# Performance work log

Hardware: AMD Instinct MI355X
Metric: run time of the kernel (lower is better)

The kernel has to match this reference:

```python
import jax, jax.numpy as jnp
import numpy as np

D_MODEL = 512
D_STATE = 16
EPS = 1e-8
LN_EPS = 1e-5


def setup_inputs() -> dict:
    key = jax.random.key(0)
    ks = jax.random.split(key, 9)
    B, N = 4, 2048
    x = jax.random.normal(ks[0], (B, N, D_MODEL), dtype=jnp.float32)
    A_log = jax.random.normal(ks[1], (D_STATE,), dtype=jnp.float32) * 0.1 - 1.0
    # xavier_uniform with gain=0.5 for B and C linear weights
    lim_B = 0.5 * np.sqrt(6.0 / (D_MODEL + D_STATE))
    W_B = jax.random.uniform(ks[2], (D_STATE, D_MODEL), jnp.float32, -lim_B, lim_B)
    W_C = jax.random.uniform(ks[3], (D_MODEL, D_STATE), jnp.float32, -lim_B, lim_B)
    D = jax.random.normal(ks[4], (D_MODEL,), dtype=jnp.float32) * 0.01
    lim_g = np.sqrt(1.0 / D_MODEL)  # torch Linear default init
    W_gate = jax.random.uniform(ks[5], (D_MODEL, D_MODEL), jnp.float32, -lim_g, lim_g)
    b_gate = jax.random.uniform(ks[6], (D_MODEL,), jnp.float32, -lim_g, lim_g)
    ln_gamma = jnp.ones((D_MODEL,), jnp.float32)
    ln_beta = jnp.zeros((D_MODEL,), jnp.float32)
    return {"x": x, "A_log": A_log, "W_B": W_B, "W_C": W_C, "D": D,
            "W_gate": W_gate, "b_gate": b_gate, "ln_gamma": ln_gamma, "ln_beta": ln_beta}


def reference(x, A_log, W_B, W_C, D, W_gate, b_gate, ln_gamma, ln_beta):
    Bb, N, Dm = x.shape
    A = -jnp.clip(jnp.exp(A_log), EPS, 10.0)                      # (d_state,)
    dt = 1.0 / N
    A_bar = jnp.exp(dt * A)                                       # (d_state,)
    B_bar = jnp.where(jnp.abs(A) > EPS, (A_bar - 1.0) / (A + EPS),
                      jnp.full_like(A, dt))
    Bu = jnp.einsum('bnm,sm->bns', x, W_B) * B_bar                # (B,N,d_state)
    idx = jnp.arange(N)
    diff = jnp.clip(idx[None, :] - idx[:, None], 0, None)[..., None]  # (N,N,1)
    decay = A_bar[None, None, :] ** diff                          # (N,N,d_state)
    mask = (idx[None, :] >= idx[:, None])[..., None]
    decay = decay * mask.astype(decay.dtype)
    h = jnp.einsum('nms,bns->bms', decay, Bu)                     # (B,N,d_state)
    h = jnp.clip(h, -10.0, 10.0)
    y = jnp.einsum('bns,ms->bnm', h, W_C) + D * x                 # (B,N,d_model)
    gate = jax.nn.sigmoid(jnp.einsum('bnm,km->bnk', x, W_gate) + b_gate)
    y = gate * y + (1.0 - gate) * x
    # LayerNorm (dropout is identity in eval mode)
    mu = jnp.mean(y, axis=-1, keepdims=True)
    var = jnp.var(y, axis=-1, keepdims=True)
    return (y - mu) / jnp.sqrt(var + LN_EPS) * ln_gamma + ln_beta
```

## Files before the change

kernel.cpp:

```cpp
#include <hip/hip_runtime.h>
#include <math.h>
#include <stdint.h>

#define D_MODEL 512
#define D_STATE 16
#define NSEQ    2048
#define NBATCH  4
#define EPSF    1e-8f
#define LN_EPSF 1e-5f
#define DT      (1.0f / 2048.0f)

typedef __attribute__((ext_vector_type(8))) short short8;
typedef __attribute__((ext_vector_type(4))) float floatx4;

__device__ __forceinline__ ushort f2bf(float f) {
    uint32_t u = __float_as_uint(f);
    return (ushort)((u + 0x7fffu + ((u >> 16) & 1u)) >> 16);
}

__global__ __launch_bounds__(256) void kP(const float* __restrict__ x,
                                          const float* __restrict__ A_log,
                                          const float* __restrict__ W_B,
                                          const float* __restrict__ Wg,
                                          ushort* __restrict__ wgb,
                                          float* __restrict__ hL,
                                          float* __restrict__ states) {
    __shared__ float wb[D_STATE][D_MODEL + 4];
    __shared__ float bbars[16], abars[16];
    __shared__ float w4[4][16];
    const int tid = threadIdx.x, lane = tid & 63, wave = tid >> 6;

    if (tid < 64) {
        int i = blockIdx.x * 64 + tid;
        const float4* sp = (const float4*)Wg + (size_t)i * 2;
        float4 a = sp[0], b = sp[1];
        float v[8] = {a.x, a.y, a.z, a.w, b.x, b.y, b.z, b.w};
        short8 o;
        #pragma unroll
        for (int j = 0; j < 8; ++j) o[j] = (short)f2bf(v[j]);
        *(short8*)(wgb + (size_t)i * 8) = o;
    }
    if (tid < 16) {
        float A    = -fminf(fmaxf(expf(A_log[tid]), EPSF), 10.0f);
        float Abar = expf(A * DT);
        abars[tid] = Abar;
        bbars[tid] = (fabsf(A) > EPSF) ? (Abar - 1.0f) / (A + EPSF) : DT;
    }
    __syncthreads();
    for (int i = tid; i < D_STATE * D_MODEL; i += 256) {
        int s = i >> 9, m = i & 511;
        wb[s][m] = W_B[i] * bbars[s];
    }
    __syncthreads();

    const int s    = lane & 15;
    const int q    = lane >> 4;
    const int rloc = q + (wave << 2);
    const int row  = blockIdx.x * 16 + rloc;
    const float* xr = x + (size_t)row * D_MODEL;

    float acc = 0.f;
    #pragma unroll 4
    for (int m = 0; m < D_MODEL; m += 4) {
        float4 xv = *(const float4*)(xr + m);
        float4 wv = *(const float4*)(&wb[s][m]);
        acc += xv.x * wv.x + xv.y * wv.y + xv.z * wv.z + xv.w * wv.w;
    }

    float abar = abars[s];
    float a = abar, b = acc;
    {
        float ap = __shfl_up(a, 16), bp = __shfl_up(b, 16);
        if (lane >= 16) { b = a * bp + b; a = a * ap; }
    }
    {
        float ap = __shfl_up(a, 32), bp = __shfl_up(b, 32);
        if (lane >= 32) { b = a * bp + b; a = a * ap; }
    }
    if (q == 3) w4[wave][s] = b;
    __syncthreads();
    float a4 = abar * abar; a4 = a4 * a4;
    float pb = 0.f;
    for (int w = 0; w < wave; ++w) pb = a4 * pb + w4[w][s];
    float hloc = a * pb + b;

    hL[(size_t)row * D_STATE + s] = hloc;
    if (rloc == 15) states[(size_t)blockIdx.x * D_STATE + s] = hloc;
}

#define CBM 16
#define BKC 64
__global__ __launch_bounds__(256) void kc_fused(
    const float*  __restrict__ x,
    const ushort* __restrict__ Wg,
    const float*  __restrict__ hL,
    const float*  __restrict__ states,
    const float*  __restrict__ A_log,
    const float*  __restrict__ W_C,
    const float*  __restrict__ Dvec,
    const float*  __restrict__ bg,
    const float*  __restrict__ gamma,
    const float*  __restrict__ beta,
    float* __restrict__ out) {
    __shared__ ushort Bsub[512 * BKC];
    __shared__ float  hsf[CBM][D_STATE];
    __shared__ float  red[4][CBM][2];

    const int tid  = threadIdx.x;
    const int lane = tid & 63, wave = tid >> 6;
    const int r0   = blockIdx.x * CBM;
    const int fr   = lane & 15, kg = lane >> 4;
    const int colw = wave * 128;

    short8 afp[8][2];
    #pragma unroll
    for (int t = 0; t < 8; ++t) {
        const float* ap = x + (size_t)(r0 + fr) * D_MODEL + t * 64 + kg * 8;
        float4 u0 = *(const float4*)ap;
        float4 u1 = *(const float4*)(ap + 4);
        float4 v0 = *(const float4*)(ap + 32);
        float4 v1 = *(const float4*)(ap + 36);
        float uu[8] = {u0.x,u0.y,u0.z,u0.w,u1.x,u1.y,u1.z,u1.w};
        float vv[8] = {v0.x,v0.y,v0.z,v0.w,v1.x,v1.y,v1.z,v1.w};
        #pragma unroll
        for (int e = 0; e < 8; ++e) {
            afp[t][0][e] = (short)f2bf(uu[e]);
            afp[t][1][e] = (short)f2bf(vv[e]);
        }
    }

    float* stg = (float*)Bsub;
    const int c0 = blockIdx.x & 127;
    for (int i = tid; i < c0 * 16; i += 256)
        stg[i] = states[(size_t)(blockIdx.x - c0) * 16 + i];
    __syncthreads();
    {
        int s = tid & 15, nloc = tid >> 4;
        float A   = -fminf(fmaxf(expf(A_log[s]), EPSF), 10.0f);
        float a16 = expf(A * DT * 16.0f);
        float p = 0.f;
        for (int cc = 0; cc < c0; ++cc) p = a16 * p + stg[cc * 16 + s];
        float hv = expf(A * DT * (float)(nloc + 1)) * p
                 + hL[(size_t)(r0 + nloc) * D_STATE + s];
        hsf[nloc][s] = fminf(fmaxf(hv, -10.f), 10.f);
    }

    floatx4 acc[8] = {};
    #pragma unroll
    for (int t = 0; t < 8; ++t) {
        __syncthreads();
        #pragma unroll
        for (int is = 0; is < 16; ++is) {
            int row_ = is * 32 + (tid >> 3);
            int g_   = (tid & 7) ^ (row_ & 7);
            const ushort* gsrc_ = Wg + (size_t)row_ * D_MODEL + t * 64 + g_ * 8;
            __builtin_amdgcn_global_load_lds(
                (const __attribute__((address_space(1))) void*)gsrc_,
                (__attribute__((address_space(3))) void*)((char*)Bsub + is * 4096 + tid * 16),
                16, 0, 0);
        }
        __syncthreads();

        #pragma unroll
        for (int j = 0; j < 8; ++j) {
            int rb = colw + j * 16 + fr;
            short8 b0 = *(const short8*)(Bsub + (size_t)rb * BKC + (((kg    ) ^ (rb & 7)) * 8));
            short8 b1 = *(const short8*)(Bsub + (size_t)rb * BKC + (((kg + 4) ^ (rb & 7)) * 8));
            acc[j] = __builtin_amdgcn_mfma_f32_16x16x32_bf16(afp[t][0], b0, acc[j], 0, 0, 0);
            acc[j] = __builtin_amdgcn_mfma_f32_16x16x32_bf16(afp[t][1], b1, acc[j], 0, 0, 0);
        }
    }

    float vsum[4] = {}, vsq[4] = {};
    #pragma unroll
    for (int j = 0; j < 8; ++j) {
        int col = colw + j * 16 + fr;
        float dv = Dvec[col], bgv = bg[col];
        const float4* wcp = (const float4*)(W_C + (size_t)col * D_STATE);
        float4 w0 = wcp[0], w1 = wcp[1], w2 = wcp[2], w3 = wcp[3];
        #pragma unroll
        for (int q = 0; q < 4; ++q) {
            int rl = kg * 4 + q;
            float xv = x[(size_t)(r0 + rl) * D_MODEL + col];
            const float* hp = hsf[rl];
            float yv = dv * xv
                + hp[0]*w0.x + hp[1]*w0.y + hp[2]*w0.z + hp[3]*w0.w
                + hp[4]*w1.x + hp[5]*w1.y + hp[6]*w1.z + hp[7]*w1.w
                + hp[8]*w2.x + hp[9]*w2.y + hp[10]*w2.z + hp[11]*w2.w
                + hp[12]*w3.x + hp[13]*w3.y + hp[14]*w3.z + hp[15]*w3.w;
            float lg = acc[j][q] + bgv;
            float gt = 1.f / (1.f + expf(-lg));
            float v  = gt * yv + (1.f - gt) * xv;
            acc[j][q] = v;
            vsum[q] += v;
            vsq[q]  += v * v;
        }
    }
    #pragma unroll
    for (int off = 1; off < 16; off <<= 1) {
        #pragma unroll
        for (int q = 0; q < 4; ++q) {
            vsum[q] += __shfl_xor(vsum[q], off);
            vsq[q]  += __shfl_xor(vsq[q], off);
        }
    }
    if (fr == 0) {
        #pragma unroll
        for (int q = 0; q < 4; ++q) {
            red[wave][kg * 4 + q][0] = vsum[q];
            red[wave][kg * 4 + q][1] = vsq[q];
        }
    }
    __syncthreads();
    float mu[4], rs[4];
    #pragma unroll
    for (int q = 0; q < 4; ++q) {
        int rl = kg * 4 + q;
        float s = 0.f, ss = 0.f;
        #pragma unroll
        for (int w = 0; w < 4; ++w) { s += red[w][rl][0]; ss += red[w][rl][1]; }
        float m   = s * (1.f / (float)D_MODEL);
        float var = ss * (1.f / (float)D_MODEL) - m * m;
        mu[q] = m;
        rs[q] = rsqrtf(var + LN_EPSF);
    }
    #pragma unroll
    for (int j = 0; j < 8; ++j) {
        int col = colw + j * 16 + fr;
        float ga = gamma[col], be = beta[col];
        #pragma unroll
        for (int q = 0; q < 4; ++q)
            out[(size_t)(r0 + kg * 4 + q) * D_MODEL + col] =
                (acc[j][q] - mu[q]) * rs[q] * ga + be;
    }
}

extern "C" void kernel_launch(void* const* d_in, const int* in_sizes, int n_in,
                              void* d_out, int out_size, void* d_ws, size_t ws_size,
                              hipStream_t stream) {
    const float* x     = (const float*)d_in[0];
    const float* A_log = (const float*)d_in[1];
    const float* W_B   = (const float*)d_in[2];
    const float* W_C   = (const float*)d_in[3];
    const float* Dv    = (const float*)d_in[4];
    const float* Wg    = (const float*)d_in[5];
    const float* bg    = (const float*)d_in[6];
    const float* gamma = (const float*)d_in[7];
    const float* beta  = (const float*)d_in[8];
    float* out = (float*)d_out;

    const int rows = NBATCH * NSEQ;

    ushort* wgb    = (ushort*)d_ws;
    float*  hL     = (float*)(wgb + (size_t)D_MODEL * D_MODEL);
    float*  states = hL + (size_t)rows * D_STATE;

    hipLaunchKernelGGL(kP, dim3(rows / 16), dim3(256), 0, stream,
                       x, A_log, W_B, Wg, wgb, hL, states);
    hipLaunchKernelGGL(kc_fused, dim3(rows / CBM), dim3(256), 0, stream,
                       x, wgb, hL, states, A_log, W_C, Dv, bg, gamma, beta, out);
}
```

Measured before the change: 58.55 us.

## Double row tile per block to share W_gate LDS tiles across 8 waves

The fused gate/LayerNorm kernel now handles 32 rows per block with 512 threads, and two groups of four waves share each W_gate bf16 tile staged in LDS. This halves the total number of W_gate tile loads from global/L2 across the grid and halves the block count. The cross-chunk state prefix and the LayerNorm reduction indexing are reworked to cover two 16-row chunks per block. In exchange there are fewer blocks (256), larger blocks with more synchronisation cost, and possibly lower occupancy.

After: 50.40 us. -13.9%, faster.

```diff
diff --git a/kernel.cpp b/kernel.cpp
--- a/kernel.cpp
+++ b/kernel.cpp
@@ -88,9 +88,9 @@
     if (rloc == 15) states[(size_t)blockIdx.x * D_STATE + s] = hloc;
 }
 
-#define CBM 16
+#define CBM 32
 #define BKC 64
-__global__ __launch_bounds__(256) void kc_fused(
+__global__ __launch_bounds__(512) void kc_fused(
     const float*  __restrict__ x,
     const ushort* __restrict__ Wg,
     const float*  __restrict__ hL,
@@ -104,18 +104,19 @@
     float* __restrict__ out) {
     __shared__ ushort Bsub[512 * BKC];
     __shared__ float  hsf[CBM][D_STATE];
-    __shared__ float  red[4][CBM][2];
+    __shared__ float  red[8][CBM][2];
 
     const int tid  = threadIdx.x;
     const int lane = tid & 63, wave = tid >> 6;
     const int r0   = blockIdx.x * CBM;
     const int fr   = lane & 15, kg = lane >> 4;
-    const int colw = wave * 128;
+    const int rbase = r0 + (wave >> 2) * 16;
+    const int colw  = (wave & 3) * 128;
 
     short8 afp[8][2];
     #pragma unroll
     for (int t = 0; t < 8; ++t) {
-        const float* ap = x + (size_t)(r0 + fr) * D_MODEL + t * 64 + kg * 8;
+        const float* ap = x + (size_t)(rbase + fr) * D_MODEL + t * 64 + kg * 8;
         float4 u0 = *(const float4*)ap;
         float4 u1 = *(const float4*)(ap + 4);
         float4 v0 = *(const float4*)(ap + 32);
@@ -130,17 +131,19 @@
     }
 
     float* stg = (float*)Bsub;
-    const int c0 = blockIdx.x & 127;
-    for (int i = tid; i < c0 * 16; i += 256)
-        stg[i] = states[(size_t)(blockIdx.x - c0) * 16 + i];
+    const int c0    = (blockIdx.x & 63) * 2;
+    const int cbase = (blockIdx.x >> 6) * 128;
+    for (int i = tid; i < (c0 + 1) * 16; i += 512)
+        stg[i] = states[(size_t)cbase * 16 + i];
     __syncthreads();
     {
         int s = tid & 15, nloc = tid >> 4;
         float A   = -fminf(fmaxf(expf(A_log[s]), EPSF), 10.0f);
         float a16 = expf(A * DT * 16.0f);
+        int nch = c0 + (nloc >> 4);
         float p = 0.f;
-        for (int cc = 0; cc < c0; ++cc) p = a16 * p + stg[cc * 16 + s];
-        float hv = expf(A * DT * (float)(nloc + 1)) * p
+        for (int cc = 0; cc < nch; ++cc) p = a16 * p + stg[cc * 16 + s];
+        float hv = expf(A * DT * (float)((nloc & 15) + 1)) * p
                  + hL[(size_t)(r0 + nloc) * D_STATE + s];
         hsf[nloc][s] = fminf(fmaxf(hv, -10.f), 10.f);
     }
@@ -150,13 +153,13 @@
     for (int t = 0; t < 8; ++t) {
         __syncthreads();
         #pragma unroll
-        for (int is = 0; is < 16; ++is) {
-            int row_ = is * 32 + (tid >> 3);
+        for (int is = 0; is < 8; ++is) {
+            int row_ = is * 64 + (tid >> 3);
             int g_   = (tid & 7) ^ (row_ & 7);
             const ushort* gsrc_ = Wg + (size_t)row_ * D_MODEL + t * 64 + g_ * 8;
             __builtin_amdgcn_global_load_lds(
                 (const __attribute__((address_space(1))) void*)gsrc_,
-                (__attribute__((address_space(3))) void*)((char*)Bsub + is * 4096 + tid * 16),
+                (__attribute__((address_space(3))) void*)((char*)Bsub + is * 8192 + tid * 16),
                 16, 0, 0);
         }
         __syncthreads();
@@ -180,9 +183,9 @@
         float4 w0 = wcp[0], w1 = wcp[1], w2 = wcp[2], w3 = wcp[3];
         #pragma unroll
         for (int q = 0; q < 4; ++q) {
-            int rl = kg * 4 + q;
-            float xv = x[(size_t)(r0 + rl) * D_MODEL + col];
-            const float* hp = hsf[rl];
+            int rloc = (wave >> 2) * 16 + kg * 4 + q;
+            float xv = x[(size_t)(r0 + rloc) * D_MODEL + col];
+            const float* hp = hsf[rloc];
             float yv = dv * xv
                 + hp[0]*w0.x + hp[1]*w0.y + hp[2]*w0.z + hp[3]*w0.w
                 + hp[4]*w1.x + hp[5]*w1.y + hp[6]*w1.z + hp[7]*w1.w
@@ -207,18 +210,23 @@
     if (fr == 0) {
         #pragma unroll
         for (int q = 0; q < 4; ++q) {
-            red[wave][kg * 4 + q][0] = vsum[q];
-            red[wave][kg * 4 + q][1] = vsq[q];
+            int rloc = (wave >> 2) * 16 + kg * 4 + q;
+            red[wave][rloc][0] = vsum[q];
+            red[wave][rloc][1] = vsq[q];
         }
     }
     __syncthreads();
     float mu[4], rs[4];
     #pragma unroll
     for (int q = 0; q < 4; ++q) {
-        int rl = kg * 4 + q;
+        int rloc = (wave >> 2) * 16 + kg * 4 + q;
+        int wg0  = (wave >> 2) * 4;
         float s = 0.f, ss = 0.f;
         #pragma unroll
-        for (int w = 0; w < 4; ++w) { s += red[w][rl][0]; ss += red[w][rl][1]; }
+        for (int w = 0; w < 4; ++w) {
+            s  += red[wg0 + w][rloc][0];
+            ss += red[wg0 + w][rloc][1];
+        }
         float m   = s * (1.f / (float)D_MODEL);
         float var = ss * (1.f / (float)D_MODEL) - m * m;
         mu[q] = m;
@@ -229,9 +237,11 @@
         int col = colw + j * 16 + fr;
         float ga = gamma[col], be = beta[col];
         #pragma unroll
-        for (int q = 0; q < 4; ++q)
-            out[(size_t)(r0 + kg * 4 + q) * D_MODEL + col] =
+        for (int q = 0; q < 4; ++q) {
+            int rloc = (wave >> 2) * 16 + kg * 4 + q;
+            out[(size_t)(r0 + rloc) * D_MODEL + col] =
                 (acc[j][q] - mu[q]) * rs[q] * ga + be;
+        }
     }
 }
 
@@ -257,6 +267,6 @@
 
     hipLaunchKernelGGL(kP, dim3(rows / 16), dim3(256), 0, stream,
                        x, A_log, W_B, Wg, wgb, hL, states);
-    hipLaunchKernelGGL(kc_fused, dim3(rows / CBM), dim3(256), 0, stream,
+    hipLaunchKernelGGL(kc_fused, dim3(rows / CBM), dim3(512), 0, stream,
                        x, wgb, hL, states, A_log, W_C, Dv, bg, gamma, beta, out);
 }
```
